# Kernel tuning notes

Hardware: AMD Instinct MI355X
Metric: run time of the kernel (lower is better)

The kernel has to match this reference:

```python
import math
import jax, jax.numpy as jnp
import numpy as np

SILU_SCALE = 1.0 / 0.6  # ScaledSiLU used in PaiNN/OCP codebases

N, E, H, F = 50000, 800000, 128, 128


def setup_inputs() -> dict:
    key = jax.random.key(0)
    ks = jax.random.split(key, 12)
    w = 0.05
    return {
        "x": jax.random.normal(ks[0], (N, H), jnp.float32),
        "vec": jax.random.normal(ks[1], (N, 3, H), jnp.float32),
        "edge_rbf": jax.random.normal(ks[2], (E, F), jnp.float32),
        "edge_vector": jax.random.normal(ks[3], (E, 3), jnp.float32),
        "edge_index": jax.random.randint(ks[4], (2, E), 0, N, dtype=jnp.int64),
        # x_proj: Linear(H, H//2) -> ScaledSiLU -> Linear(H//2, 3H)
        "W1": jax.random.normal(ks[5], (H, H // 2), jnp.float32) * w,
        "b1": jax.random.normal(ks[6], (H // 2,), jnp.float32) * w,
        "W2": jax.random.normal(ks[7], (H // 2, 3 * H), jnp.float32) * w,
        "b2": jax.random.normal(ks[8], (3 * H,), jnp.float32) * w,
        # edge_proj: Linear(F, 3H)
        "We": jax.random.normal(ks[9], (F, 3 * H), jnp.float32) * w,
        "be": jax.random.normal(ks[10], (3 * H,), jnp.float32) * w,
    }


def reference(x, vec, edge_rbf, edge_vector, W1, b1, W2, b2, We, be, edge_index):
    n_nodes, hidden = x.shape
    inv_sqrt_3 = 1.0 / math.sqrt(3.0)
    inv_sqrt_h = 1.0 / math.sqrt(hidden)

    j, i = edge_index[0], edge_index[1]

    rbf_h = edge_rbf @ We + be                      # [E, 3H]
    h = jax.nn.silu(x @ W1 + b1) * SILU_SCALE       # [N, H/2]
    x_h = h @ W2 + b2                               # [N, 3H]

    xm = x_h[j] * rbf_h * inv_sqrt_3                # [E, 3H] gather + fuse
    x_ji1, x_ji2, x_ji3 = jnp.split(xm, 3, axis=-1)  # each [E, H]

    # [E,1,H]*[E,3,H] + [E,1,H]*[E,3,1] -> [E,3,H]
    vec_ji = (x_ji1[:, None, :] * vec[j]
              + x_ji2[:, None, :] * edge_vector[:, :, None]) * inv_sqrt_h

    d_vec = jax.ops.segment_sum(vec_ji, i, num_segments=n_nodes)  # [N,3,H]
    d_x = jax.ops.segment_sum(x_ji3, i, num_segments=n_nodes)     # [N,H]
    return (d_x, d_vec)
```

## Files before the change

kernel.cpp:

```cpp
#include <hip/hip_runtime.h>
#include <hip/hip_bf16.h>
#include <math.h>

#define N_NODES 50000
#define N_EDGES 800000
#define HID 128
#define NF 128
#define C3 384
#define SILU_SCALE (1.0f/0.6f)
#define INV_SQRT3 0.57735026918962576f
#define INV_SQRTH 0.08838834764831845f

#define GMAX 96880
#define GBLOCKS (GMAX / 4)
#define PERM_SLOTS (GMAX * 16)

typedef __bf16 bf16x8 __attribute__((ext_vector_type(8)));
typedef __bf16 bf16x4 __attribute__((ext_vector_type(4)));
typedef float  floatx4 __attribute__((ext_vector_type(4)));

__global__ void cast_weT(const float* __restrict__ We, __bf16* __restrict__ WeT) {
    int o = blockIdx.x * 256 + threadIdx.x;
    int n = o / NF, k = o % NF;
    WeT[o] = (__bf16)We[k * C3 + n];
}

__global__ __launch_bounds__(384)
void node_mlp(const float* __restrict__ x,  const float* __restrict__ W1,
              const float* __restrict__ b1, const float* __restrict__ W2,
              const float* __restrict__ b2, float* __restrict__ x_h) {
    __shared__ float xs[16][HID];
    __shared__ float hs[16][64];
    const int t = threadIdx.x;
    const int base = blockIdx.x * 16;

    for (int f4 = t; f4 < 512; f4 += 384) {
        float4 v = ((const float4*)(x + (size_t)base * HID))[f4];
        ((float4*)&xs[0][0])[f4] = v;
    }
    __syncthreads();
    for (int o = t; o < 1024; o += 384) {
        int g = o >> 6, m = o & 63;
        float sum = b1[m];
        #pragma unroll 8
        for (int k = 0; k < HID; ++k) sum += xs[g][k] * W1[k * 64 + m];
        float sig = 1.0f / (1.0f + __expf(-sum));
        hs[g][m] = sum * sig * SILU_SCALE;
    }
    __syncthreads();
    {
        float acc[16];
        #pragma unroll
        for (int n = 0; n < 16; ++n) acc[n] = b2[t];
        for (int k = 0; k < 64; ++k) {
            float w2 = W2[k * C3 + t];
            #pragma unroll
            for (int n = 0; n < 16; ++n) acc[n] += hs[n][k] * w2;
        }
        #pragma unroll
        for (int n = 0; n < 16; ++n) x_h[(size_t)(base + n) * C3 + t] = acc[n];
    }
}

__global__ void hist_k(const int* __restrict__ eidx, int* __restrict__ counts) {
    int e = blockIdx.x * 256 + threadIdx.x;
    if (e < N_EDGES) atomicAdd(&counts[eidx[N_EDGES + e]], 1);
}

__global__ __launch_bounds__(1024)
void scan_k(const int* __restrict__ counts, int* __restrict__ first_group,
            int* __restrict__ group_node, int* __restrict__ group_valid,
            int* __restrict__ G_total) {
    __shared__ int ls[1024];
    const int t = threadIdx.x;
    const int CH = 49;
    const int base = t * CH;
    int s = 0;
    for (int k = 0; k < CH; ++k) {
        int i = base + k;
        if (i < N_NODES) s += (counts[i] + 15) >> 4;
    }
    ls[t] = s;
    __syncthreads();
    for (int off = 1; off < 1024; off <<= 1) {
        int v = (t >= off) ? ls[t - off] : 0;
        __syncthreads();
        ls[t] += v;
        __syncthreads();
    }
    if (t == 1023) *G_total = ls[1023];
    int run = (t == 0) ? 0 : ls[t - 1];
    for (int k = 0; k < CH; ++k) {
        int i = base + k;
        if (i < N_NODES) {
            int d = counts[i];
            int ng = (d + 15) >> 4;
            first_group[i] = run;
            for (int q = 0; q < ng; ++q) {
                group_node[run + q]  = i;
                int rem = d - 16 * q;
                group_valid[run + q] = rem > 16 ? 16 : rem;
            }
            run += ng;
        }
    }
}

__global__ void scatter_k(const int* __restrict__ eidx,
                          const int* __restrict__ first_group,
                          int* __restrict__ cursor, int* __restrict__ perm) {
    int e = blockIdx.x * 256 + threadIdx.x;
    if (e >= N_EDGES) return;
    int i = eidx[N_EDGES + e];
    int pos = atomicAdd(&cursor[i], 1);
    perm[first_group[i] * 16 + pos] = e;
}

__global__ __launch_bounds__(256)
void edge_kernel(const float* __restrict__ edge_rbf,
                 const __bf16* __restrict__ WeT,
                 const float* __restrict__ be,
                 const float* __restrict__ x_h,
                 const float* __restrict__ vec,
                 const float* __restrict__ edge_vector,
                 const int*   __restrict__ eidx,
                 const int*   __restrict__ perm,
                 const int*   __restrict__ group_node,
                 const int*   __restrict__ group_valid,
                 const int*   __restrict__ G_total,
                 float* __restrict__ d_x, float* __restrict__ d_vec) {
    __shared__ __bf16 Ash[64][136];
    __shared__ int perm_s[64];
    const int t = threadIdx.x;
    const int g0 = blockIdx.x * 4;

    if (t < 64) perm_s[t] = perm[(size_t)g0 * 16 + t];
    __syncthreads();

    #pragma unroll
    for (int it = 0; it < 8; ++it) {
        int fidx = it * 256 + t;
        int row  = fidx >> 5;
        int c4   = fidx & 31;
        const float4 v = *(const float4*)(edge_rbf + (size_t)perm_s[row] * NF + c4 * 4);
        bf16x4 b;
        b[0] = (__bf16)v.x; b[1] = (__bf16)v.y; b[2] = (__bf16)v.z; b[3] = (__bf16)v.w;
        *(bf16x4*)&Ash[row][c4 * 4] = b;
    }
    __syncthreads();

    const int w = t >> 6, l = t & 63;
    const int er = l & 15, quad = l >> 4;
    const int g = g0 + w;
    if (g >= *G_total) return;

    const int i_node = group_node[g];
    const int nval   = group_valid[g];

    bf16x8 afrag[4];
    #pragma unroll
    for (int s = 0; s < 4; ++s)
        afrag[s] = *(const bf16x8*)&Ash[16 * w + er][s * 32 + quad * 8];

    int jj[4]; float ev0[4], ev1[4], ev2[4];
    #pragma unroll
    for (int r = 0; r < 4; ++r) {
        int e = perm_s[16 * w + quad * 4 + r];
        jj[r]  = eidx[e];
        ev0[r] = edge_vector[(size_t)e * 3 + 0];
        ev1[r] = edge_vector[(size_t)e * 3 + 1];
        ev2[r] = edge_vector[(size_t)e * 3 + 2];
    }

    float* dxp = d_x  + (size_t)i_node * HID;
    float* dvp = d_vec + (size_t)i_node * 3 * HID;

    #pragma unroll
    for (int ct = 0; ct < 8; ++ct) {
        floatx4 a1 = (floatx4){0.f,0.f,0.f,0.f};
        floatx4 a2 = (floatx4){0.f,0.f,0.f,0.f};
        floatx4 a3 = (floatx4){0.f,0.f,0.f,0.f};
        #pragma unroll
        for (int s = 0; s < 4; ++s) {
            const __bf16* bb = WeT + (size_t)(16 * ct + er) * NF + s * 32 + quad * 8;
            a1 = __builtin_amdgcn_mfma_f32_16x16x32_bf16(afrag[s], *(const bf16x8*)bb, a1, 0, 0, 0);
            a2 = __builtin_amdgcn_mfma_f32_16x16x32_bf16(afrag[s], *(const bf16x8*)(bb + 128 * NF), a2, 0, 0, 0);
            a3 = __builtin_amdgcn_mfma_f32_16x16x32_bf16(afrag[s], *(const bf16x8*)(bb + 256 * NF), a3, 0, 0, 0);
        }
        const int cc = ct * 16 + er;
        const float be1 = be[cc], be2 = be[cc + 128], be3 = be[cc + 256];
        float p0 = 0.f, p1 = 0.f, p2 = 0.f, p3 = 0.f;
        #pragma unroll
        for (int r = 0; r < 4; ++r) {
            const float* xh = x_h + (size_t)jj[r] * C3;
            const float* vj = vec + (size_t)jj[r] * 3 * HID;
            float rbf1 = a1[r] + be1;
            float rbf2 = a2[r] + be2;
            float rbf3 = a3[r] + be3;
            float x1 = xh[cc]       * rbf1 * INV_SQRT3;
            float x2 = xh[cc + 128] * rbf2 * INV_SQRT3;
            float x3 = xh[cc + 256] * rbf3 * INV_SQRT3;
            if ((quad * 4 + r) >= nval) { x1 = 0.f; x2 = 0.f; x3 = 0.f; }
            p0 += x3;
            p1 += x1 * vj[cc]       + x2 * ev0[r];
            p2 += x1 * vj[cc + 128] + x2 * ev1[r];
            p3 += x1 * vj[cc + 256] + x2 * ev2[r];
        }
        p0 += __shfl_xor(p0, 16, 64); p0 += __shfl_xor(p0, 32, 64);
        p1 += __shfl_xor(p1, 16, 64); p1 += __shfl_xor(p1, 32, 64);
        p2 += __shfl_xor(p2, 16, 64); p2 += __shfl_xor(p2, 32, 64);
        p3 += __shfl_xor(p3, 16, 64); p3 += __shfl_xor(p3, 32, 64);
        if (quad == (ct & 3)) {
            unsafeAtomicAdd(dxp + cc, p0);
            unsafeAtomicAdd(dvp + cc,       p1 * INV_SQRTH);
            unsafeAtomicAdd(dvp + cc + 128, p2 * INV_SQRTH);
            unsafeAtomicAdd(dvp + cc + 256, p3 * INV_SQRTH);
        }
    }
}

extern "C" void kernel_launch(void* const* d_in, const int* in_sizes, int n_in,
                              void* d_out, int out_size, void* d_ws, size_t ws_size,
                              hipStream_t stream) {
    const float* x    = (const float*)d_in[0];
    const float* vec  = (const float*)d_in[1];
    const float* erbf = (const float*)d_in[2];
    const float* evec = (const float*)d_in[3];
    const int*   eidx = (const int*)d_in[4];
    const float* W1   = (const float*)d_in[5];
    const float* b1   = (const float*)d_in[6];
    const float* W2   = (const float*)d_in[7];
    const float* b2   = (const float*)d_in[8];
    const float* We   = (const float*)d_in[9];
    const float* be   = (const float*)d_in[10];

    float* out   = (float*)d_out;
    float* d_x   = out;
    float* d_vec = out + (size_t)N_NODES * HID;

    char* p = (char*)d_ws;
    float*  x_h        = (float*)p;  p += (size_t)N_NODES * C3 * 4;
    __bf16* WeT        = (__bf16*)p; p += (size_t)C3 * NF * 2;
    int* first_group   = (int*)p;    p += 50176 * 4;
    int* group_node    = (int*)p;    p += (GMAX + 16) * 4;
    int* group_valid   = (int*)p;    p += (GMAX + 16) * 4;
    int* G_total       = (int*)p;    p += 256;
    char* zbase        = p;
    int* counts        = (int*)p;    p += 50176 * 4;
    int* cursor        = (int*)p;    p += 50176 * 4;
    int* perm          = (int*)p;    p += (size_t)PERM_SLOTS * 4;
    size_t zbytes      = (size_t)(p - zbase);

    hipMemsetAsync(zbase, 0, zbytes, stream);
    hipMemsetAsync(d_out, 0, (size_t)out_size * sizeof(float), stream);

    cast_weT<<<(C3 * NF) / 256, 256, 0, stream>>>(We, WeT);
    node_mlp<<<N_NODES / 16, 384, 0, stream>>>(x, W1, b1, W2, b2, x_h);
    hist_k<<<(N_EDGES + 255) / 256, 256, 0, stream>>>(eidx, counts);
    scan_k<<<1, 1024, 0, stream>>>(counts, first_group, group_node, group_valid, G_total);
    scatter_k<<<(N_EDGES + 255) / 256, 256, 0, stream>>>(eidx, first_group, cursor, perm);
    edge_kernel<<<GBLOCKS, 256, 0, stream>>>(erbf, WeT, be, x_h, vec, evec, eidx,
                                             perm, group_node, group_valid, G_total,
                                             d_x, d_vec);
}
```

Baseline: 1.907 ms.

## Store gathered node features in bf16, transpose MFMA layout, parallelize group fill

```diff
diff --git a/kernel.cpp b/kernel.cpp
--- a/kernel.cpp
+++ b/kernel.cpp
@@ -25,10 +25,18 @@
     WeT[o] = (__bf16)We[k * C3 + n];
 }
 
+__global__ void cast_vec(const float* __restrict__ v, __bf16* __restrict__ vb) {
+    int o = blockIdx.x * 256 + threadIdx.x;
+    float4 u = ((const float4*)v)[o];
+    bf16x4 b;
+    b[0] = (__bf16)u.x; b[1] = (__bf16)u.y; b[2] = (__bf16)u.z; b[3] = (__bf16)u.w;
+    ((bf16x4*)vb)[o] = b;
+}
+
 __global__ __launch_bounds__(384)
 void node_mlp(const float* __restrict__ x,  const float* __restrict__ W1,
               const float* __restrict__ b1, const float* __restrict__ W2,
-              const float* __restrict__ b2, float* __restrict__ x_h) {
+              const float* __restrict__ b2, __bf16* __restrict__ x_hb) {
     __shared__ float xs[16][HID];
     __shared__ float hs[16][64];
     const int t = threadIdx.x;
@@ -58,7 +66,7 @@
             for (int n = 0; n < 16; ++n) acc[n] += hs[n][k] * w2;
         }
         #pragma unroll
-        for (int n = 0; n < 16; ++n) x_h[(size_t)(base + n) * C3 + t] = acc[n];
+        for (int n = 0; n < 16; ++n) x_hb[(size_t)(base + n) * C3 + t] = (__bf16)acc[n];
     }
 }
 
@@ -69,7 +77,6 @@
 
 __global__ __launch_bounds__(1024)
 void scan_k(const int* __restrict__ counts, int* __restrict__ first_group,
-            int* __restrict__ group_node, int* __restrict__ group_valid,
             int* __restrict__ G_total) {
     __shared__ int ls[1024];
     const int t = threadIdx.x;
@@ -93,16 +100,22 @@
     for (int k = 0; k < CH; ++k) {
         int i = base + k;
         if (i < N_NODES) {
-            int d = counts[i];
-            int ng = (d + 15) >> 4;
             first_group[i] = run;
-            for (int q = 0; q < ng; ++q) {
-                group_node[run + q]  = i;
-                int rem = d - 16 * q;
-                group_valid[run + q] = rem > 16 ? 16 : rem;
-            }
-            run += ng;
-        }
+            run += (counts[i] + 15) >> 4;
+        }
+    }
+}
+
+__global__ void fill_k(const int* __restrict__ counts,
+                       const int* __restrict__ first_group,
+                       int* __restrict__ group_node, int* __restrict__ group_valid) {
+    int i = blockIdx.x * 256 + threadIdx.x;
+    if (i >= N_NODES) return;
+    int d = counts[i], fg = first_group[i], ng = (d + 15) >> 4;
+    for (int q = 0; q < ng; ++q) {
+        group_node[fg + q]  = i;
+        int rem = d - 16 * q;
+        group_valid[fg + q] = rem > 16 ? 16 : rem;
     }
 }
 
@@ -120,8 +133,8 @@
 void edge_kernel(const float* __restrict__ edge_rbf,
                  const __bf16* __restrict__ WeT,
                  const float* __restrict__ be,
-                 const float* __restrict__ x_h,
-                 const float* __restrict__ vec,
+                 const __bf16* __restrict__ x_hb,
+                 const __bf16* __restrict__ vecb,
                  const float* __restrict__ edge_vector,
                  const int*   __restrict__ eidx,
                  const int*   __restrict__ perm,
@@ -129,49 +142,36 @@
                  const int*   __restrict__ group_valid,
                  const int*   __restrict__ G_total,
                  float* __restrict__ d_x, float* __restrict__ d_vec) {
-    __shared__ __bf16 Ash[64][136];
-    __shared__ int perm_s[64];
     const int t = threadIdx.x;
-    const int g0 = blockIdx.x * 4;
-
-    if (t < 64) perm_s[t] = perm[(size_t)g0 * 16 + t];
-    __syncthreads();
-
-    #pragma unroll
-    for (int it = 0; it < 8; ++it) {
-        int fidx = it * 256 + t;
-        int row  = fidx >> 5;
-        int c4   = fidx & 31;
-        const float4 v = *(const float4*)(edge_rbf + (size_t)perm_s[row] * NF + c4 * 4);
-        bf16x4 b;
-        b[0] = (__bf16)v.x; b[1] = (__bf16)v.y; b[2] = (__bf16)v.z; b[3] = (__bf16)v.w;
-        *(bf16x4*)&Ash[row][c4 * 4] = b;
-    }
-    __syncthreads();
-
     const int w = t >> 6, l = t & 63;
     const int er = l & 15, quad = l >> 4;
-    const int g = g0 + w;
+    const int g = blockIdx.x * 4 + w;
     if (g >= *G_total) return;
 
     const int i_node = group_node[g];
     const int nval   = group_valid[g];
-
-    bf16x8 afrag[4];
+    const int e      = perm[(size_t)g * 16 + er];
+    const int j      = eidx[e];
+    const float ev0  = edge_vector[(size_t)e * 3 + 0];
+    const float ev1  = edge_vector[(size_t)e * 3 + 1];
+    const float ev2  = edge_vector[(size_t)e * 3 + 2];
+    const float sA   = (er < nval) ? INV_SQRT3 : 0.f;
+    const float sB   = sA * INV_SQRTH;
+
+    bf16x8 bfrag[4];
+    const float* rp = edge_rbf + (size_t)e * NF + quad * 8;
     #pragma unroll
-    for (int s = 0; s < 4; ++s)
-        afrag[s] = *(const bf16x8*)&Ash[16 * w + er][s * 32 + quad * 8];
-
-    int jj[4]; float ev0[4], ev1[4], ev2[4];
-    #pragma unroll
-    for (int r = 0; r < 4; ++r) {
-        int e = perm_s[16 * w + quad * 4 + r];
-        jj[r]  = eidx[e];
-        ev0[r] = edge_vector[(size_t)e * 3 + 0];
-        ev1[r] = edge_vector[(size_t)e * 3 + 1];
-        ev2[r] = edge_vector[(size_t)e * 3 + 2];
-    }
-
+    for (int s = 0; s < 4; ++s) {
+        const float4 u0 = *(const float4*)(rp + s * 32);
+        const float4 u1 = *(const float4*)(rp + s * 32 + 4);
+        bf16x8 b;
+        b[0] = (__bf16)u0.x; b[1] = (__bf16)u0.y; b[2] = (__bf16)u0.z; b[3] = (__bf16)u0.w;
+        b[4] = (__bf16)u1.x; b[5] = (__bf16)u1.y; b[6] = (__bf16)u1.z; b[7] = (__bf16)u1.w;
+        bfrag[s] = b;
+    }
+
+    const __bf16* xh = x_hb + (size_t)j * C3;
+    const __bf16* vj = vecb + (size_t)j * C3;
     float* dxp = d_x  + (size_t)i_node * HID;
     float* dvp = d_vec + (size_t)i_node * 3 * HID;
 
@@ -180,41 +180,58 @@
         floatx4 a1 = (floatx4){0.f,0.f,0.f,0.f};
         floatx4 a2 = (floatx4){0.f,0.f,0.f,0.f};
         floatx4 a3 = (floatx4){0.f,0.f,0.f,0.f};
+        const __bf16* wp = WeT + (size_t)(16 * ct + er) * NF + quad * 8;
         #pragma unroll
         for (int s = 0; s < 4; ++s) {
-            const __bf16* bb = WeT + (size_t)(16 * ct + er) * NF + s * 32 + quad * 8;
-            a1 = __builtin_amdgcn_mfma_f32_16x16x32_bf16(afrag[s], *(const bf16x8*)bb, a1, 0, 0, 0);
-            a2 = __builtin_amdgcn_mfma_f32_16x16x32_bf16(afrag[s], *(const bf16x8*)(bb + 128 * NF), a2, 0, 0, 0);
-            a3 = __builtin_amdgcn_mfma_f32_16x16x32_bf16(afrag[s], *(const bf16x8*)(bb + 256 * NF), a3, 0, 0, 0);
-        }
-        const int cc = ct * 16 + er;
-        const float be1 = be[cc], be2 = be[cc + 128], be3 = be[cc + 256];
-        float p0 = 0.f, p1 = 0.f, p2 = 0.f, p3 = 0.f;
+            a1 = __builtin_amdgcn_mfma_f32_16x16x32_bf16(*(const bf16x8*)(wp + s * 32),            bfrag[s], a1, 0, 0, 0);
+            a2 = __builtin_amdgcn_mfma_f32_16x16x32_bf16(*(const bf16x8*)(wp + 128 * NF + s * 32), bfrag[s], a2, 0, 0, 0);
+            a3 = __builtin_amdgcn_mfma_f32_16x16x32_bf16(*(const bf16x8*)(wp + 256 * NF + s * 32), bfrag[s], a3, 0, 0, 0);
+        }
+        const int c0 = ct * 16 + quad * 4;
+        const bf16x4 xh1 = *(const bf16x4*)(xh + c0);
+        const bf16x4 xh2 = *(const bf16x4*)(xh + 128 + c0);
+        const bf16x4 xh3 = *(const bf16x4*)(xh + 256 + c0);
+        const bf16x4 vj0 = *(const bf16x4*)(vj + c0);
+        const bf16x4 vj1 = *(const bf16x4*)(vj + 128 + c0);
+        const bf16x4 vj2 = *(const bf16x4*)(vj + 256 + c0);
+        const float4 be1 = *(const float4*)(be + c0);
+        const float4 be2 = *(const float4*)(be + 128 + c0);
+        const float4 be3 = *(const float4*)(be + 256 + c0);
+        float q0[4], q1[4], q2[4], q3[4];
+        const float* be1p = (const float*)&be1;
+        const float* be2p = (const float*)&be2;
+        const float* be3p = (const float*)&be3;
         #pragma unroll
         for (int r = 0; r < 4; ++r) {
-            const float* xh = x_h + (size_t)jj[r] * C3;
-            const float* vj = vec + (size_t)jj[r] * 3 * HID;
-            float rbf1 = a1[r] + be1;
-            float rbf2 = a2[r] + be2;
-            float rbf3 = a3[r] + be3;
-            float x1 = xh[cc]       * rbf1 * INV_SQRT3;
-            float x2 = xh[cc + 128] * rbf2 * INV_SQRT3;
-            float x3 = xh[cc + 256] * rbf3 * INV_SQRT3;
-            if ((quad * 4 + r) >= nval) { x1 = 0.f; x2 = 0.f; x3 = 0.f; }
-            p0 += x3;
-            p1 += x1 * vj[cc]       + x2 * ev0[r];
-            p2 += x1 * vj[cc + 128] + x2 * ev1[r];
-            p3 += x1 * vj[cc + 256] + x2 * ev2[r];
-        }
-        p0 += __shfl_xor(p0, 16, 64); p0 += __shfl_xor(p0, 32, 64);
-        p1 += __shfl_xor(p1, 16, 64); p1 += __shfl_xor(p1, 32, 64);
-        p2 += __shfl_xor(p2, 16, 64); p2 += __shfl_xor(p2, 32, 64);
-        p3 += __shfl_xor(p3, 16, 64); p3 += __shfl_xor(p3, 32, 64);
-        if (quad == (ct & 3)) {
-            unsafeAtomicAdd(dxp + cc, p0);
-            unsafeAtomicAdd(dvp + cc,       p1 * INV_SQRTH);
-            unsafeAtomicAdd(dvp + cc + 128, p2 * INV_SQRTH);
-            unsafeAtomicAdd(dvp + cc + 256, p3 * INV_SQRTH);
+            const float rbf1 = a1[r] + be1p[r];
+            const float rbf2 = a2[r] + be2p[r];
+            const float rbf3 = a3[r] + be3p[r];
+            const float x1 = (float)xh1[r] * rbf1 * sB;
+            const float x2 = (float)xh2[r] * rbf2 * sB;
+            const float x3 = (float)xh3[r] * rbf3 * sA;
+            q0[r] = x3;
+            q1[r] = x1 * (float)vj0[r] + x2 * ev0;
+            q2[r] = x1 * (float)vj1[r] + x2 * ev1;
+            q3[r] = x1 * (float)vj2[r] + x2 * ev2;
+        }
+        #pragma unroll
+        for (int m = 1; m <= 8; m <<= 1) {
+            #pragma unroll
+            for (int r = 0; r < 4; ++r) {
+                q0[r] += __shfl_xor(q0[r], m);
+                q1[r] += __shfl_xor(q1[r], m);
+                q2[r] += __shfl_xor(q2[r], m);
+                q3[r] += __shfl_xor(q3[r], m);
+            }
+        }
+        if (er < 4) {
+            float* bp = (er == 0) ? (dxp + c0) : (dvp + (er - 1) * HID + c0);
+            #pragma unroll
+            for (int r = 0; r < 4; ++r) {
+                const float v = (er == 0) ? q0[r] : (er == 1) ? q1[r]
+                              : (er == 2) ? q2[r] : q3[r];
+                unsafeAtomicAdd(bp + r, v);
+            }
         }
     }
 }
@@ -239,7 +256,8 @@
     float* d_vec = out + (size_t)N_NODES * HID;
 
     char* p = (char*)d_ws;
-    float*  x_h        = (float*)p;  p += (size_t)N_NODES * C3 * 4;
+    __bf16* x_hb       = (__bf16*)p; p += (size_t)N_NODES * C3 * 2;
+    __bf16* vecb       = (__bf16*)p; p += (size_t)N_NODES * C3 * 2;
     __bf16* WeT        = (__bf16*)p; p += (size_t)C3 * NF * 2;
     int* first_group   = (int*)p;    p += 50176 * 4;
     int* group_node    = (int*)p;    p += (GMAX + 16) * 4;
@@ -255,11 +273,14 @@
     hipMemsetAsync(d_out, 0, (size_t)out_size * sizeof(float), stream);
 
     cast_weT<<<(C3 * NF) / 256, 256, 0, stream>>>(We, WeT);
-    node_mlp<<<N_NODES / 16, 384, 0, stream>>>(x, W1, b1, W2, b2, x_h);
+    cast_vec<<<(N_NODES * 3 * HID / 4) / 256, 256, 0, stream>>>(vec, vecb);
+    node_mlp<<<N_NODES / 16, 384, 0, stream>>>(x, W1, b1, W2, b2, x_hb);
     hist_k<<<(N_EDGES + 255) / 256, 256, 0, stream>>>(eidx, counts);
-    scan_k<<<1, 1024, 0, stream>>>(counts, first_group, group_node, group_valid, G_total);
+    scan_k<<<1, 1024, 0, stream>>>(counts, first_group, G_total);
+    fill_k<<<(N_NODES + 255) / 256, 256, 0, stream>>>(counts, first_group,
+                                                      group_node, group_valid);
     scatter_k<<<(N_EDGES + 255) / 256, 256, 0, stream>>>(eidx, first_group, cursor, perm);
-    edge_kernel<<<GBLOCKS, 256, 0, stream>>>(erbf, WeT, be, x_h, vec, evec, eidx,
+    edge_kernel<<<GBLOCKS, 256, 0, stream>>>(erbf, WeT, be, x_hb, vecb, evec, eidx,
                                              perm, group_node, group_valid, G_total,
                                              d_x, d_vec);
 }
```

Result: slower. 2.096 ms (+9.9%).
